# Kernel optimization log

Hardware: AMD Instinct MI355X
Metric: run time of the kernel (lower is better)

The kernel has to match this reference:

```python
import jax, jax.numpy as jnp
import numpy as np

EPS = 1e-5

def _layer_norm(x, g, b):
    mu = jnp.mean(x, axis=-1, keepdims=True)
    var = jnp.mean((x - mu) ** 2, axis=-1, keepdims=True)
    return (x - mu) * jax.lax.rsqrt(var + EPS) * g + b

def _aggregate(x, ei, emask):
    # x: [N, D], ei: [2, E], emask: [E] (0/1 float). Mean over valid incoming edges.
    N = x.shape[0]
    src, tgt = ei[0], ei[1]
    valid = emask > 0
    tgt_eff = jnp.where(valid, tgt, N)  # route masked edges to dummy segment
    msgs = x[src] * emask[:, None]      # [E, D]
    sums = jax.ops.segment_sum(msgs, tgt_eff, num_segments=N + 1)[:N]
    cnt = jax.ops.segment_sum(emask, tgt_eff, num_segments=N + 1)[:N]
    return sums / jnp.maximum(cnt, 1.0)[:, None]

def _forward(node_feats, edge_index, node_mask, edge_mask,
             in_W, in_b, self_W, self_b, neigh_W, neigh_b, ln_g, ln_b,
             out1_W, out1_b, out2_W, out2_b):
    x = jax.nn.relu(node_feats @ in_W + in_b)  # [B, N, H]
    L = self_W.shape[0]
    agg_fn = jax.vmap(_aggregate)
    for l in range(L):
        self_feats = x @ self_W[l] + self_b[l]
        neigh = agg_fn(x, edge_index, edge_mask)
        neigh_feats = neigh @ neigh_W[l] + neigh_b[l]
        h = jax.nn.relu(self_feats + neigh_feats)
        h = _layer_norm(h, ln_g[l], ln_b[l])
        x = h * node_mask[:, :, None]
    # global mean_max pool
    masked = x * node_mask[:, :, None]
    n_valid = jnp.maximum(jnp.sum(node_mask, axis=1, keepdims=True), 1.0)
    mean_pool = jnp.sum(masked, axis=1) / n_valid
    neg_inf = jnp.asarray(-jnp.inf, x.dtype)
    max_pool = jnp.max(jnp.where(node_mask[:, :, None] > 0, masked, neg_inf), axis=1)
    g = jnp.concatenate([mean_pool, max_pool], axis=1)  # [B, 2H]
    h = jax.nn.relu(g @ out1_W + out1_b)
    return h @ out2_W + out2_b  # [B, output_dim]

def setup_inputs() -> dict:
    key = jax.random.key(0)
    ks = jax.random.split(key, 12)
    B, N, E = 8, 8192, 65536
    F_IN, H, OUT, L = 64, 128, 256, 3
    inp = {}
    inp['graph_node_feats'] = jax.random.normal(ks[0], (B, N, F_IN), jnp.float32)
    inp['graph_edge_index'] = jax.random.randint(ks[1], (B, 2, E), 0, N, jnp.int32)
    inp['graph_node_mask'] = jnp.ones((B, N), jnp.float32)
    inp['graph_edge_mask'] = jnp.ones((B, E), jnp.float32)
    s = lambda k, sh, fan: jax.random.normal(k, sh, jnp.float32) * (1.0 / np.sqrt(fan))
    inp['in_W'] = s(ks[2], (F_IN, H), F_IN)
    inp['in_b'] = jnp.zeros((H,), jnp.float32)
    inp['self_W'] = s(ks[3], (L, H, H), H)
    inp['self_b'] = jnp.zeros((L, H), jnp.float32)
    inp['neigh_W'] = s(ks[4], (L, H, H), H)
    inp['neigh_b'] = jnp.zeros((L, H), jnp.float32)
    inp['ln_g'] = jnp.ones((L, H), jnp.float32)
    inp['ln_b'] = jnp.zeros((L, H), jnp.float32)
    inp['out1_W'] = s(ks[5], (2 * H, H), 2 * H)
    inp['out1_b'] = jnp.zeros((H,), jnp.float32)
    inp['out2_W'] = s(ks[6], (H, OUT), H)
    inp['out2_b'] = jnp.zeros((OUT,), jnp.float32)
    return inp

def reference(graph_node_feats, graph_edge_index, graph_node_mask, graph_edge_mask,
              in_W, in_b, self_W, self_b, neigh_W, neigh_b, ln_g, ln_b,
              out1_W, out1_b, out2_W, out2_b):
    return _forward(graph_node_feats, graph_edge_index, graph_node_mask, graph_edge_mask,
                    in_W, in_b, self_W, self_b, neigh_W, neigh_b, ln_g, ln_b,
                    out1_W, out1_b, out2_W, out2_b)
```

## Files before the change

kernel.cpp:

```cpp
#include <hip/hip_runtime.h>
#include <hip/hip_bf16.h>

#define B 8
#define N 8192
#define E 65536
#define FIN 64
#define H 128
#define OUTD 256
#define NLAYER 3
#define EPS 1e-5f
#define NCHUNK 128
#define NNODE (B * N)
#define KSTEPS 8
#define BPL (KSTEPS * 8 * 512)
#define INSTEPS 6
#define ELLW 48

#define AS1 __attribute__((address_space(1)))
#define AS3 __attribute__((address_space(3)))

typedef float f32x4 __attribute__((ext_vector_type(4)));
typedef __bf16 bf16x8 __attribute__((ext_vector_type(8)));

__device__ __forceinline__ float b2f(unsigned short u) {
    union { float f; unsigned int i; } c; c.i = ((unsigned int)u) << 16; return c.f;
}
__device__ __forceinline__ unsigned short f2b(float f) {
    __hip_bfloat16 h = __float2bfloat16(f);
    return *reinterpret_cast<unsigned short*>(&h);
}

__global__ void k_prep(const float* __restrict__ selfW, const float* __restrict__ neighW,
                       const float* __restrict__ inW,
                       unsigned short* __restrict__ Bp, unsigned short* __restrict__ Bpi) {
    const int idx = blockIdx.x;
    const int lane = threadIdx.x;
    const int quad = lane >> 4, col = lane & 15;
    if (idx < NLAYER * KSTEPS * 8) {
        const int t = idx & 7;
        const int s = (idx >> 3) % KSTEPS;
        const int l = idx / (KSTEPS * 8);
        const int g = s >> 2;
        const float* W = ((g == 0) ? selfW : neighW) + (size_t)l * H * H;
        const int n = t * 16 + col;
        unsigned short* dst = Bp + ((size_t)(l * KSTEPS + s) * 8 + t) * 512 + lane * 8;
        #pragma unroll
        for (int j = 0; j < 8; ++j) {
            const int kk = (s & 3) * 32 + quad * 8 + j;
            dst[j] = f2b(W[kk * H + n]);
        }
    } else {
        const int idx2 = idx - NLAYER * KSTEPS * 8;
        const int t = idx2 & 7;
        const int s = idx2 >> 3;
        const int g = s >> 1;
        const bool lo = (g == 2);
        const int n = t * 16 + col;
        unsigned short* dst = Bpi + ((size_t)(s * 8 + t)) * 512 + lane * 8;
        #pragma unroll
        for (int j = 0; j < 8; ++j) {
            const int kk = (s & 1) * 32 + quad * 8 + j;
            const float w = inW[kk * H + n];
            const unsigned short hi = f2b(w);
            dst[j] = lo ? f2b(w - b2f(hi)) : hi;
        }
    }
}

__global__ __launch_bounds__(256) void k_front(const float* __restrict__ feats,
                                               const unsigned short* __restrict__ Bpi,
                                               const float* __restrict__ bias,
                                               unsigned short* __restrict__ xh,
                                               const int* __restrict__ ei,
                                               const float* __restrict__ emask,
                                               int* __restrict__ ecnt,
                                               unsigned int* __restrict__ ell) {
    const int tid = threadIdx.x;
    if (blockIdx.x >= 1024) {
        const int ge = (blockIdx.x - 1024) * 256 + tid;
        const float m = emask[ge];
        if (m > 0.f) {
            const int b = ge >> 16, e = ge & 0xFFFF;
            const int tgt = ei[(b * 2 + 1) * E + e];
            const int src = ei[(b * 2) * E + e];
            const int r = b * N + tgt;
            const int p = atomicAdd(&ecnt[r], 1);
            if (p < ELLW)
                ell[(size_t)r * ELLW + p] = ((unsigned int)f2b(m) << 16) | (unsigned int)src;
        }
        return;
    }
    const int wv = tid >> 6, lane = tid & 63;
    const int quad = lane >> 4, col = lane & 15;
    const int mg = wv >> 1, nw = wv & 1;
    const int row0 = blockIdx.x * 64;

    bf16x8 fh[2][2], fl[2][2];
    #pragma unroll
    for (int mt = 0; mt < 2; ++mt) {
        const int row = row0 + (mg * 2 + mt) * 16 + col;
        #pragma unroll
        for (int j = 0; j < 2; ++j) {
            const float* src = &feats[(size_t)row * FIN + j * 32 + quad * 8];
            const float4 v0 = *(const float4*)src;
            const float4 v1 = *(const float4*)(src + 4);
            const float fv[8] = {v0.x, v0.y, v0.z, v0.w, v1.x, v1.y, v1.z, v1.w};
            union { bf16x8 v; unsigned short u[8]; } Hh, Ll;
            #pragma unroll
            for (int q = 0; q < 8; ++q) {
                const unsigned short hu = f2b(fv[q]);
                Hh.u[q] = hu;
                Ll.u[q] = f2b(fv[q] - b2f(hu));
            }
            fh[mt][j] = Hh.v;
            fl[mt][j] = Ll.v;
        }
    }

    f32x4 acc[2][4] = {};
    bf16x8 bC[4];
    #pragma unroll
    for (int nt = 0; nt < 4; ++nt)
        bC[nt] = *(const bf16x8*)&Bpi[((size_t)(nw * 4 + nt)) * 512 + lane * 8];

    #pragma unroll
    for (int s = 0; s < INSTEPS; ++s) {
        bf16x8 bN[4];
        if (s + 1 < INSTEPS) {
            #pragma unroll
            for (int nt = 0; nt < 4; ++nt)
                bN[nt] = *(const bf16x8*)&Bpi[((size_t)(s + 1) * 8 + nw * 4 + nt) * 512 + lane * 8];
        }
        const int g = s >> 1, j = s & 1;
        #pragma unroll
        for (int mt = 0; mt < 2; ++mt) {
            const bf16x8 a = (g == 1) ? fl[mt][j] : fh[mt][j];
            #pragma unroll
            for (int nt = 0; nt < 4; ++nt)
                acc[mt][nt] = __builtin_amdgcn_mfma_f32_16x16x32_bf16(a, bC[nt], acc[mt][nt], 0, 0, 0);
        }
        #pragma unroll
        for (int nt = 0; nt < 4; ++nt) bC[nt] = bN[nt];
    }

    #pragma unroll
    for (int nt = 0; nt < 4; ++nt) {
        const int hh = (nw * 4 + nt) * 16 + col;
        const float bv = bias[hh];
        #pragma unroll
        for (int mt = 0; mt < 2; ++mt)
            #pragma unroll
            for (int r = 0; r < 4; ++r) {
                const int row = row0 + (mg * 2 + mt) * 16 + quad * 4 + r;
                const float y = fmaxf(acc[mt][nt][r] + bv, 0.f);
                xh[(size_t)row * H + hh] = f2b(y);
            }
    }
}

__global__ __launch_bounds__(256) void k_gather7(const unsigned int* __restrict__ xh32,
                                                 const int* __restrict__ ecnt,
                                                 const unsigned int* __restrict__ ell,
                                                 unsigned int* __restrict__ nh32) {
    const int beta = blockIdx.x;
    const int b = beta & 7;
    const int grp = beta >> 3;
    const int wave = threadIdx.x >> 6, lane = threadIdx.x & 63;
    const int r = b * N + grp * 4 + wave;
    unsigned int pv = 0;
    if (lane < ELLW) pv = ell[(size_t)r * ELLW + lane];
    const int cnt = min(ecnt[r], ELLW);
    if (lane >= cnt) pv = 0;
    const size_t bbase = (size_t)b * N * 64;
    float a0 = 0.f, a1 = 0.f, c = 0.f;
    const int cnt8 = (cnt + 7) & ~7;
    for (int jj = 0; jj < cnt8; jj += 8) {
        #pragma unroll
        for (int q = 0; q < 8; ++q) {
            const unsigned int pk = __shfl(pv, jj + q);
            const float m = b2f((unsigned short)(pk >> 16));
            const unsigned int u = xh32[bbase + (size_t)(pk & 0xFFFFu) * 64 + lane];
            union { unsigned int i; float f; } lo, hi;
            lo.i = u << 16;
            hi.i = u & 0xFFFF0000u;
            a0 = fmaf(lo.f, m, a0);
            a1 = fmaf(hi.f, m, a1);
            c += m;
        }
    }
    const float inv = 1.f / fmaxf(c, 1.f);
    nh32[(size_t)r * 64 + lane] = (unsigned int)f2b(a0 * inv) | ((unsigned int)f2b(a1 * inv) << 16);
}

__global__ __launch_bounds__(256) void k_layer9(const unsigned short* __restrict__ xinh,
                                                const unsigned short* __restrict__ nh,
                                                const unsigned short* __restrict__ Bp,
                                                const float* __restrict__ sb,
                                                const float* __restrict__ nb,
                                                const float* __restrict__ lng,
                                                const float* __restrict__ lnb,
                                                const float* __restrict__ nmask,
                                                unsigned short* __restrict__ oxh,
                                                float* __restrict__ part,
                                                const int last) {
    __shared__ __align__(16) unsigned short bbuf[2][16 * 512];
    __shared__ float lsum[2][64];
    __shared__ float lsq[2][64];
    __shared__ float psum_s[2][H];
    __shared__ float pmax_s[2][H];

    const int tid = threadIdx.x;
    const int wv = tid >> 6, lane = tid & 63;
    const int quad = lane >> 4, col = lane & 15;
    const int mg = wv >> 1, nw = wv & 1;
    const int u = blockIdx.x;
    const int b = u & 7;
    const int chunk = u >> 3;
    const int row0 = b * N + chunk * 64;

    size_t abase[2];
    #pragma unroll
    for (int mt = 0; mt < 2; ++mt)
        abase[mt] = (size_t)(row0 + (mg * 2 + mt) * 16 + col) * H + quad * 8;

    #pragma unroll
    for (int i = 0; i < 4; ++i) {
        const unsigned short* g = Bp + (size_t)(wv * 4 + i) * 512 + lane * 8;
        __builtin_amdgcn_global_load_lds((const AS1 unsigned int*)g,
                                         (AS3 unsigned int*)&bbuf[0][(wv * 4 + i) * 512],
                                         16, 0, 0);
    }
    bf16x8 aC[2][2];
    #pragma unroll
    for (int j = 0; j < 2; ++j)
        #pragma unroll
        for (int mt = 0; mt < 2; ++mt)
            aC[j][mt] = *(const bf16x8*)&xinh[abase[mt] + j * 32];

    f32x4 acc[2][4] = {};

    #pragma unroll
    for (int c = 0; c < 4; ++c) {
        __syncthreads();
        bf16x8 aN[2][2];
        if (c < 3) {
            const int c1 = c + 1;
            #pragma unroll
            for (int i = 0; i < 4; ++i) {
                const unsigned short* g = Bp + (size_t)(c1 * 16 + wv * 4 + i) * 512 + lane * 8;
                __builtin_amdgcn_global_load_lds((const AS1 unsigned int*)g,
                                                 (AS3 unsigned int*)&bbuf[c1 & 1][(wv * 4 + i) * 512],
                                                 16, 0, 0);
            }
            const unsigned short* A1 = (c1 < 2) ? xinh : nh;
            #pragma unroll
            for (int j = 0; j < 2; ++j)
                #pragma unroll
                for (int mt = 0; mt < 2; ++mt)
                    aN[j][mt] = *(const bf16x8*)&A1[abase[mt] + ((c1 & 1) * 2 + j) * 32];
        }
        #pragma unroll
        for (int j = 0; j < 2; ++j) {
            bf16x8 bf[4];
            #pragma unroll
            for (int nt = 0; nt < 4; ++nt)
                bf[nt] = *(const bf16x8*)&bbuf[c & 1][(j * 8 + nw * 4 + nt) * 512 + lane * 8];
            #pragma unroll
            for (int mt = 0; mt < 2; ++mt)
                #pragma unroll
                for (int nt = 0; nt < 4; ++nt)
                    acc[mt][nt] = __builtin_amdgcn_mfma_f32_16x16x32_bf16(aC[j][mt], bf[nt], acc[mt][nt], 0, 0, 0);
        }
        #pragma unroll
        for (int j = 0; j < 2; ++j)
            #pragma unroll
            for (int mt = 0; mt < 2; ++mt)
                aC[j][mt] = aN[j][mt];
    }

    float sbv[4], nbv[4], gv[4], bbv[4];
    #pragma unroll
    for (int nt = 0; nt < 4; ++nt) {
        const int hh = (nw * 4 + nt) * 16 + col;
        sbv[nt] = sb[hh]; nbv[nt] = nb[hh]; gv[nt] = lng[hh]; bbv[nt] = lnb[hh];
    }
    #pragma unroll
    for (int mt = 0; mt < 2; ++mt)
        #pragma unroll
        for (int nt = 0; nt < 4; ++nt)
            #pragma unroll
            for (int r = 0; r < 4; ++r)
                acc[mt][nt][r] = fmaxf(acc[mt][nt][r] + sbv[nt] + nbv[nt], 0.f);

    #pragma unroll
    for (int mt = 0; mt < 2; ++mt)
        #pragma unroll
        for (int r = 0; r < 4; ++r) {
            float p = 0.f, q = 0.f;
            #pragma unroll
            for (int nt = 0; nt < 4; ++nt) {
                const float v = acc[mt][nt][r];
                p += v;
                q = fmaf(v, v, q);
            }
            p += __shfl_xor(p, 1);  q += __shfl_xor(q, 1);
            p += __shfl_xor(p, 2);  q += __shfl_xor(q, 2);
            p += __shfl_xor(p, 4);  q += __shfl_xor(q, 4);
            p += __shfl_xor(p, 8);  q += __shfl_xor(q, 8);
            if (col == 0) {
                const int rib = (mg * 2 + mt) * 16 + quad * 4 + r;
                lsum[nw][rib] = p;
                lsq[nw][rib] = q;
            }
        }
    __syncthreads();

    float psum[4] = {0.f, 0.f, 0.f, 0.f};
    float pmax[4] = {-INFINITY, -INFINITY, -INFINITY, -INFINITY};

    #pragma unroll
    for (int mt = 0; mt < 2; ++mt)
        #pragma unroll
        for (int r = 0; r < 4; ++r) {
            const int rib = (mg * 2 + mt) * 16 + quad * 4 + r;
            const int node = row0 + rib;
            const float mu = (lsum[0][rib] + lsum[1][rib]) * (1.f / H);
            const float var = (lsq[0][rib] + lsq[1][rib]) * (1.f / H) - mu * mu;
            const float isd = rsqrtf(var + EPS);
            const float m = nmask[node];
            #pragma unroll
            for (int nt = 0; nt < 4; ++nt) {
                const float y = (fmaf(acc[mt][nt][r] - mu, isd * gv[nt], bbv[nt])) * m;
                if (!last) {
                    oxh[(size_t)node * H + (nw * 4 + nt) * 16 + col] = f2b(y);
                } else {
                    psum[nt] += y;
                    pmax[nt] = fmaxf(pmax[nt], (m > 0.f) ? y : -INFINITY);
                }
            }
        }

    if (last) {
        #pragma unroll
        for (int nt = 0; nt < 4; ++nt) {
            psum[nt] += __shfl_xor(psum[nt], 16);
            psum[nt] += __shfl_xor(psum[nt], 32);
            pmax[nt] = fmaxf(pmax[nt], __shfl_xor(pmax[nt], 16));
            pmax[nt] = fmaxf(pmax[nt], __shfl_xor(pmax[nt], 32));
        }
        if (quad == 0)
            #pragma unroll
            for (int nt = 0; nt < 4; ++nt) {
                psum_s[mg][(nw * 4 + nt) * 16 + col] = psum[nt];
                pmax_s[mg][(nw * 4 + nt) * 16 + col] = pmax[nt];
            }
        float nv = 0.f;
        if (wv == 0) {
            nv = nmask[row0 + lane];
            nv += __shfl_xor(nv, 1);  nv += __shfl_xor(nv, 2);
            nv += __shfl_xor(nv, 4);  nv += __shfl_xor(nv, 8);
            nv += __shfl_xor(nv, 16); nv += __shfl_xor(nv, 32);
        }
        __syncthreads();
        float* p = part + ((size_t)b * NCHUNK + chunk) * (2 * H + 1);
        if (tid < H) {
            p[tid] = psum_s[0][tid] + psum_s[1][tid];
            p[H + tid] = fmaxf(pmax_s[0][tid], pmax_s[1][tid]);
        }
        if (tid == 0) p[2 * H] = nv;
    }
}

__global__ __launch_bounds__(1024) void k_tail2(const float* __restrict__ part,
                                                const float* __restrict__ W1, const float* __restrict__ b1,
                                                const float* __restrict__ W2, const float* __restrict__ b2,
                                                float* __restrict__ out) {
    const int b = blockIdx.x, tid = threadIdx.x;
    const int col = tid & 255;
    const int sub = tid >> 8;
    __shared__ float sred[4][2 * H];
    __shared__ float nvl[NCHUNK];
    __shared__ float g[2 * H];
    __shared__ float hid[H];

    {
        float acc = (col < H) ? 0.f : -INFINITY;
        #pragma unroll 8
        for (int c = sub * (NCHUNK / 4); c < (sub + 1) * (NCHUNK / 4); ++c) {
            const float v = part[((size_t)b * NCHUNK + c) * (2 * H + 1) + col];
            acc = (col < H) ? (acc + v) : fmaxf(acc, v);
        }
        sred[sub][col] = acc;
    }
    if (tid < NCHUNK)
        nvl[tid] = part[((size_t)b * NCHUNK + tid) * (2 * H + 1) + 2 * H];
    __syncthreads();
    for (int s = NCHUNK / 2; s > 0; s >>= 1) {
        if (tid < s) nvl[tid] += nvl[tid + s];
        __syncthreads();
    }
    const float nv = fmaxf(nvl[0], 1.f);
    if (tid < 2 * H) {
        if (tid < H)
            g[tid] = (sred[0][tid] + sred[1][tid] + sred[2][tid] + sred[3][tid]) / nv;
        else
            g[tid] = fmaxf(fmaxf(sred[0][tid], sred[1][tid]), fmaxf(sred[2][tid], sred[3][tid]));
    }
    __syncthreads();
    if (tid < H) {
        float a = b1[tid];
        #pragma unroll 8
        for (int k = 0; k < 2 * H; ++k) a = fmaf(g[k], W1[k * H + tid], a);
        hid[tid] = fmaxf(a, 0.f);
    }
    __syncthreads();
    if (tid < OUTD) {
        float a = b2[tid];
        #pragma unroll 8
        for (int k = 0; k < H; ++k) a = fmaf(hid[k], W2[k * OUTD + tid], a);
        out[(size_t)b * OUTD + tid] = a;
    }
}

extern "C" void kernel_launch(void* const* d_in, const int* in_sizes, int n_in,
                              void* d_out, int out_size, void* d_ws, size_t ws_size,
                              hipStream_t stream) {
    const float* feats = (const float*)d_in[0];
    const int*   ei    = (const int*)d_in[1];
    const float* nmask = (const float*)d_in[2];
    const float* emask = (const float*)d_in[3];
    const float* inW   = (const float*)d_in[4];
    const float* inb   = (const float*)d_in[5];
    const float* selfW = (const float*)d_in[6];
    const float* selfb = (const float*)d_in[7];
    const float* neighW= (const float*)d_in[8];
    const float* neighb= (const float*)d_in[9];
    const float* lng   = (const float*)d_in[10];
    const float* lnb   = (const float*)d_in[11];
    const float* W1    = (const float*)d_in[12];
    const float* b1    = (const float*)d_in[13];
    const float* W2    = (const float*)d_in[14];
    const float* b2    = (const float*)d_in[15];
    float* out = (float*)d_out;

    const size_t nxh = (size_t)NNODE * H;
    char* w = (char*)d_ws;
    unsigned short* xh  = (unsigned short*)w;  w += nxh * 2;
    unsigned short* nh  = (unsigned short*)w;  w += nxh * 2;
    unsigned short* Bp  = (unsigned short*)w;  w += (size_t)NLAYER * BPL * 2;
    unsigned short* Bpi = (unsigned short*)w;  w += (size_t)INSTEPS * 8 * 512 * 2;
    float* part = (float*)w;                   w += (size_t)B * NCHUNK * (2 * H + 1) * 4;
    int* ecnt   = (int*)w;                     w += (size_t)NNODE * 4;
    unsigned int* ell = (unsigned int*)w;      w += (size_t)NNODE * ELLW * 4;

    k_prep<<<NLAYER * KSTEPS * 8 + INSTEPS * 8, 64, 0, stream>>>(selfW, neighW, inW, Bp, Bpi);
    hipMemsetAsync(ecnt, 0, (size_t)NNODE * sizeof(int), stream);
    k_front<<<1024 + B * E / 256, 256, 0, stream>>>(feats, Bpi, inb, xh, ei, emask, ecnt, ell);

    for (int l = 0; l < NLAYER; ++l) {
        k_gather7<<<NNODE / 4, 256, 0, stream>>>((const unsigned int*)xh, ecnt, ell,
                                                 (unsigned int*)nh);
        k_layer9<<<NNODE / 64, 256, 0, stream>>>(xh, nh,
                                                 Bp + (size_t)l * BPL,
                                                 selfb + (size_t)l * H, neighb + (size_t)l * H,
                                                 lng + (size_t)l * H, lnb + (size_t)l * H,
                                                 nmask, xh, part, (l == NLAYER - 1) ? 1 : 0);
    }

    k_tail2<<<B, 1024, 0, stream>>>(part, W1, b1, W2, b2, out);
}
```

Before: 253.1 us.

## Fuse whole GNN pipeline into one persistent cooperative kernel with grid syncs

Replaces the separate prep, front, per-layer gather and layer kernels and the tail kernel with one cooperative persistent kernel. Work items are assigned to blocks with grid-stride loops, and phases are separated by grid.sync. The aim is to remove kernel launch gaps and the memset. In exchange it adds grid-wide barrier cost, caps occupancy through launch bounds, and serialises the front GEMM and ELL build inside each block; the old multi-kernel path stays as a fallback.

Result: slower. 906.6 us (+258.2%).

```diff
diff --git a/kernel.cpp b/kernel.cpp
--- a/kernel.cpp
+++ b/kernel.cpp
@@ -1,5 +1,8 @@
 #include <hip/hip_runtime.h>
 #include <hip/hip_bf16.h>
+#include <hip/hip_cooperative_groups.h>
+
+namespace cg = cooperative_groups;
 
 #define B 8
 #define N 8192
@@ -30,6 +33,366 @@
     return *reinterpret_cast<unsigned short*>(&h);
 }
 
+struct MegaArgs {
+    const float *feats; const int *ei; const float *nmask; const float *emask;
+    const float *inW, *inb, *selfW, *selfb, *neighW, *neighb, *lng, *lnb;
+    const float *W1, *b1, *W2, *b2;
+    float *out;
+    unsigned short *xh, *nh, *Bp, *Bpi;
+    float *part, *part2;
+    int *ecnt; unsigned int *ell;
+};
+
+__global__ __launch_bounds__(256, 4) void k_mega(MegaArgs A) {
+    cg::grid_group grid = cg::this_grid();
+    __shared__ __align__(16) unsigned short bbuf[2][16 * 512];
+    __shared__ float lsum[2][64], lsq[2][64];
+    __shared__ float psum_s[2][H], pmax_s[2][H];
+
+    const int bid = blockIdx.x, tid = threadIdx.x, GD = gridDim.x;
+    const int wv = tid >> 6, lane = tid & 63;
+    const int quad = lane >> 4, col = lane & 15;
+
+    for (int i = bid * 256 + tid; i < NNODE; i += GD * 256) A.ecnt[i] = 0;
+    for (int u4 = bid; u4 < 60; u4 += GD) {
+        const int idx = u4 * 4 + wv;
+        if (idx < NLAYER * KSTEPS * 8) {
+            const int t = idx & 7;
+            const int s = (idx >> 3) % KSTEPS;
+            const int l = idx / (KSTEPS * 8);
+            const float* W = (((s >> 2) == 0) ? A.selfW : A.neighW) + (size_t)l * H * H;
+            const int n = t * 16 + col;
+            unsigned short* dst = A.Bp + ((size_t)(l * KSTEPS + s) * 8 + t) * 512 + lane * 8;
+            #pragma unroll
+            for (int j = 0; j < 8; ++j)
+                dst[j] = f2b(W[((s & 3) * 32 + quad * 8 + j) * H + n]);
+        } else {
+            const int idx2 = idx - NLAYER * KSTEPS * 8;
+            const int t = idx2 & 7;
+            const int s = idx2 >> 3;
+            const bool lo = ((s >> 1) == 2);
+            const int n = t * 16 + col;
+            unsigned short* dst = A.Bpi + ((size_t)(s * 8 + t)) * 512 + lane * 8;
+            #pragma unroll
+            for (int j = 0; j < 8; ++j) {
+                const float w = A.inW[((s & 1) * 32 + quad * 8 + j) * H + n];
+                const unsigned short hi = f2b(w);
+                dst[j] = lo ? f2b(w - b2f(hi)) : hi;
+            }
+        }
+    }
+    grid.sync();
+
+    for (int u = bid; u < NNODE / 64; u += GD) {
+        const int mg = wv >> 1, nw = wv & 1;
+        const int row0 = u * 64;
+        bf16x8 fh[2][2], fl[2][2];
+        #pragma unroll
+        for (int mt = 0; mt < 2; ++mt) {
+            const int row = row0 + (mg * 2 + mt) * 16 + col;
+            #pragma unroll
+            for (int j = 0; j < 2; ++j) {
+                const float* src = &A.feats[(size_t)row * FIN + j * 32 + quad * 8];
+                const float4 v0 = *(const float4*)src;
+                const float4 v1 = *(const float4*)(src + 4);
+                const float fv[8] = {v0.x, v0.y, v0.z, v0.w, v1.x, v1.y, v1.z, v1.w};
+                union { bf16x8 v; unsigned short u16[8]; } Hh, Ll;
+                #pragma unroll
+                for (int q = 0; q < 8; ++q) {
+                    const unsigned short hu = f2b(fv[q]);
+                    Hh.u16[q] = hu;
+                    Ll.u16[q] = f2b(fv[q] - b2f(hu));
+                }
+                fh[mt][j] = Hh.v;
+                fl[mt][j] = Ll.v;
+            }
+        }
+        f32x4 acc[2][4] = {};
+        bf16x8 bC[4];
+        #pragma unroll
+        for (int nt = 0; nt < 4; ++nt)
+            bC[nt] = *(const bf16x8*)&A.Bpi[((size_t)(nw * 4 + nt)) * 512 + lane * 8];
+        #pragma unroll
+        for (int s = 0; s < INSTEPS; ++s) {
+            bf16x8 bN[4];
+            if (s + 1 < INSTEPS) {
+                #pragma unroll
+                for (int nt = 0; nt < 4; ++nt)
+                    bN[nt] = *(const bf16x8*)&A.Bpi[((size_t)(s + 1) * 8 + nw * 4 + nt) * 512 + lane * 8];
+            }
+            const int g = s >> 1, j = s & 1;
+            #pragma unroll
+            for (int mt = 0; mt < 2; ++mt) {
+                const bf16x8 a = (g == 1) ? fl[mt][j] : fh[mt][j];
+                #pragma unroll
+                for (int nt = 0; nt < 4; ++nt)
+                    acc[mt][nt] = __builtin_amdgcn_mfma_f32_16x16x32_bf16(a, bC[nt], acc[mt][nt], 0, 0, 0);
+            }
+            #pragma unroll
+            for (int nt = 0; nt < 4; ++nt) bC[nt] = bN[nt];
+        }
+        #pragma unroll
+        for (int nt = 0; nt < 4; ++nt) {
+            const int hh = (nw * 4 + nt) * 16 + col;
+            const float bv = A.inb[hh];
+            #pragma unroll
+            for (int mt = 0; mt < 2; ++mt)
+                #pragma unroll
+                for (int r = 0; r < 4; ++r) {
+                    const int row = row0 + (mg * 2 + mt) * 16 + quad * 4 + r;
+                    A.xh[(size_t)row * H + hh] = f2b(fmaxf(acc[mt][nt][r] + bv, 0.f));
+                }
+        }
+    }
+    for (int u = bid; u < (B * E) / 256; u += GD) {
+        const int ge = u * 256 + tid;
+        const float m = A.emask[ge];
+        if (m > 0.f) {
+            const int b = ge >> 16, e = ge & 0xFFFF;
+            const int tgt = A.ei[(b * 2 + 1) * E + e];
+            const int src = A.ei[(b * 2) * E + e];
+            const int r = b * N + tgt;
+            const int p = atomicAdd(&A.ecnt[r], 1);
+            if (p < ELLW)
+                A.ell[(size_t)r * ELLW + p] = ((unsigned int)f2b(m) << 16) | (unsigned int)src;
+        }
+    }
+    grid.sync();
+
+    const unsigned int* xh32 = (const unsigned int*)A.xh;
+    unsigned int* nh32 = (unsigned int*)A.nh;
+    for (int l = 0; l < NLAYER; ++l) {
+        for (int q = bid; q < NNODE / 4; q += GD) {
+            const int b = q & 7;
+            const int r = b * N + (q >> 3) * 4 + wv;
+            unsigned int pv = 0;
+            if (lane < ELLW) pv = A.ell[(size_t)r * ELLW + lane];
+            const int cnt = min(A.ecnt[r], ELLW);
+            if (lane >= cnt) pv = 0;
+            const size_t bbase = (size_t)b * N * 64;
+            float a0 = 0.f, a1 = 0.f, c = 0.f;
+            const int cnt8 = (cnt + 7) & ~7;
+            for (int jj = 0; jj < cnt8; jj += 8) {
+                #pragma unroll
+                for (int qq = 0; qq < 8; ++qq) {
+                    const unsigned int pk = __shfl(pv, jj + qq);
+                    const float m = b2f((unsigned short)(pk >> 16));
+                    const unsigned int uu = xh32[bbase + (size_t)(pk & 0xFFFFu) * 64 + lane];
+                    union { unsigned int i; float f; } lo, hi;
+                    lo.i = uu << 16;
+                    hi.i = uu & 0xFFFF0000u;
+                    a0 = fmaf(lo.f, m, a0);
+                    a1 = fmaf(hi.f, m, a1);
+                    c += m;
+                }
+            }
+            const float inv = 1.f / fmaxf(c, 1.f);
+            nh32[(size_t)r * 64 + lane] = (unsigned int)f2b(a0 * inv) | ((unsigned int)f2b(a1 * inv) << 16);
+        }
+        grid.sync();
+
+        const unsigned short* Bpl = A.Bp + (size_t)l * BPL;
+        const float* sb = A.selfb + l * H;
+        const float* nb = A.neighb + l * H;
+        const float* lg = A.lng + l * H;
+        const float* lb = A.lnb + l * H;
+        const int last = (l == NLAYER - 1);
+        for (int u = bid; u < NNODE / 64; u += GD) {
+            const int mg = wv >> 1, nw = wv & 1;
+            const int b = u & 7;
+            const int chunk = u >> 3;
+            const int row0 = b * N + chunk * 64;
+            size_t abase[2];
+            #pragma unroll
+            for (int mt = 0; mt < 2; ++mt)
+                abase[mt] = (size_t)(row0 + (mg * 2 + mt) * 16 + col) * H + quad * 8;
+            #pragma unroll
+            for (int i = 0; i < 4; ++i) {
+                const unsigned short* g = Bpl + (size_t)(wv * 4 + i) * 512 + lane * 8;
+                __builtin_amdgcn_global_load_lds((const AS1 unsigned int*)g,
+                                                 (AS3 unsigned int*)&bbuf[0][(wv * 4 + i) * 512],
+                                                 16, 0, 0);
+            }
+            bf16x8 aC[2][2];
+            #pragma unroll
+            for (int j = 0; j < 2; ++j)
+                #pragma unroll
+                for (int mt = 0; mt < 2; ++mt)
+                    aC[j][mt] = *(const bf16x8*)&A.xh[abase[mt] + j * 32];
+            f32x4 acc[2][4] = {};
+            #pragma unroll
+            for (int c = 0; c < 4; ++c) {
+                __syncthreads();
+                bf16x8 aN[2][2];
+                if (c < 3) {
+                    const int c1 = c + 1;
+                    #pragma unroll
+                    for (int i = 0; i < 4; ++i) {
+                        const unsigned short* g = Bpl + (size_t)(c1 * 16 + wv * 4 + i) * 512 + lane * 8;
+                        __builtin_amdgcn_global_load_lds((const AS1 unsigned int*)g,
+                                                         (AS3 unsigned int*)&bbuf[c1 & 1][(wv * 4 + i) * 512],
+                                                         16, 0, 0);
+                    }
+                    const unsigned short* A1 = (c1 < 2) ? A.xh : A.nh;
+                    #pragma unroll
+                    for (int j = 0; j < 2; ++j)
+                        #pragma unroll
+                        for (int mt = 0; mt < 2; ++mt)
+                            aN[j][mt] = *(const bf16x8*)&A1[abase[mt] + ((c1 & 1) * 2 + j) * 32];
+                }
+                #pragma unroll
+                for (int j = 0; j < 2; ++j) {
+                    bf16x8 bf[4];
+                    #pragma unroll
+                    for (int nt = 0; nt < 4; ++nt)
+                        bf[nt] = *(const bf16x8*)&bbuf[c & 1][(j * 8 + nw * 4 + nt) * 512 + lane * 8];
+                    #pragma unroll
+                    for (int mt = 0; mt < 2; ++mt)
+                        #pragma unroll
+                        for (int nt = 0; nt < 4; ++nt)
+                            acc[mt][nt] = __builtin_amdgcn_mfma_f32_16x16x32_bf16(aC[j][mt], bf[nt], acc[mt][nt], 0, 0, 0);
+                }
+                #pragma unroll
+                for (int j = 0; j < 2; ++j)
+                    #pragma unroll
+                    for (int mt = 0; mt < 2; ++mt)
+                        aC[j][mt] = aN[j][mt];
+            }
+            float sbv[4], nbv[4], gv[4], bbv[4];
+            #pragma unroll
+            for (int nt = 0; nt < 4; ++nt) {
+                const int hh = (nw * 4 + nt) * 16 + col;
+                sbv[nt] = sb[hh]; nbv[nt] = nb[hh]; gv[nt] = lg[hh]; bbv[nt] = lb[hh];
+            }
+            #pragma unroll
+            for (int mt = 0; mt < 2; ++mt)
+                #pragma unroll
+                for (int nt = 0; nt < 4; ++nt)
+                    #pragma unroll
+                    for (int r = 0; r < 4; ++r)
+                        acc[mt][nt][r] = fmaxf(acc[mt][nt][r] + sbv[nt] + nbv[nt], 0.f);
+            #pragma unroll
+            for (int mt = 0; mt < 2; ++mt)
+                #pragma unroll
+                for (int r = 0; r < 4; ++r) {
+                    float p = 0.f, q = 0.f;
+                    #pragma unroll
+                    for (int nt = 0; nt < 4; ++nt) {
+                        const float v = acc[mt][nt][r];
+                        p += v;
+                        q = fmaf(v, v, q);
+                    }
+                    p += __shfl_xor(p, 1);  q += __shfl_xor(q, 1);
+                    p += __shfl_xor(p, 2);  q += __shfl_xor(q, 2);
+                    p += __shfl_xor(p, 4);  q += __shfl_xor(q, 4);
+                    p += __shfl_xor(p, 8);  q += __shfl_xor(q, 8);
+                    if (col == 0) {
+                        const int rib = (mg * 2 + mt) * 16 + quad * 4 + r;
+                        lsum[nw][rib] = p;
+                        lsq[nw][rib] = q;
+                    }
+                }
+            __syncthreads();
+            float psum[4] = {0.f, 0.f, 0.f, 0.f};
+            float pmax[4] = {-INFINITY, -INFINITY, -INFINITY, -INFINITY};
+            #pragma unroll
+            for (int mt = 0; mt < 2; ++mt)
+                #pragma unroll
+                for (int r = 0; r < 4; ++r) {
+                    const int rib = (mg * 2 + mt) * 16 + quad * 4 + r;
+                    const int node = row0 + rib;
+                    const float mu = (lsum[0][rib] + lsum[1][rib]) * (1.f / H);
+                    const float var = (lsq[0][rib] + lsq[1][rib]) * (1.f / H) - mu * mu;
+                    const float isd = rsqrtf(var + EPS);
+                    const float m = A.nmask[node];
+                    #pragma unroll
+                    for (int nt = 0; nt < 4; ++nt) {
+                        const float y = (fmaf(acc[mt][nt][r] - mu, isd * gv[nt], bbv[nt])) * m;
+                        if (!last) {
+                            A.xh[(size_t)node * H + (nw * 4 + nt) * 16 + col] = f2b(y);
+                        } else {
+                            psum[nt] += y;
+                            pmax[nt] = fmaxf(pmax[nt], (m > 0.f) ? y : -INFINITY);
+                        }
+                    }
+                }
+            if (last) {
+                #pragma unroll
+                for (int nt = 0; nt < 4; ++nt) {
+                    psum[nt] += __shfl_xor(psum[nt], 16);
+                    psum[nt] += __shfl_xor(psum[nt], 32);
+                    pmax[nt] = fmaxf(pmax[nt], __shfl_xor(pmax[nt], 16));
+                    pmax[nt] = fmaxf(pmax[nt], __shfl_xor(pmax[nt], 32));
+                }
+                if (quad == 0)
+                    #pragma unroll
+                    for (int nt = 0; nt < 4; ++nt) {
+                        psum_s[mg][(nw * 4 + nt) * 16 + col] = psum[nt];
+                        pmax_s[mg][(nw * 4 + nt) * 16 + col] = pmax[nt];
+                    }
+                float nv = 0.f;
+                if (wv == 0) {
+                    nv = A.nmask[row0 + lane];
+                    nv += __shfl_xor(nv, 1);  nv += __shfl_xor(nv, 2);
+                    nv += __shfl_xor(nv, 4);  nv += __shfl_xor(nv, 8);
+                    nv += __shfl_xor(nv, 16); nv += __shfl_xor(nv, 32);
+                }
+                __syncthreads();
+                float* p = A.part + ((size_t)b * NCHUNK + chunk) * (2 * H + 1);
+                if (tid < H) {
+                    p[tid] = psum_s[0][tid] + psum_s[1][tid];
+                    p[H + tid] = fmaxf(pmax_s[0][tid], pmax_s[1][tid]);
+                }
+                if (tid == 0) p[2 * H] = nv;
+            }
+        }
+        grid.sync();
+    }
+
+    if (bid < 32) {
+        const int b = bid >> 2, sub = bid & 3;
+        float acc = (tid < H) ? 0.f : -INFINITY;
+        float nv = 0.f;
+        for (int c = sub * (NCHUNK / 4); c < (sub + 1) * (NCHUNK / 4); ++c) {
+            const float* p = A.part + ((size_t)b * NCHUNK + c) * (2 * H + 1);
+            if (tid < H) acc += p[tid];
+            else acc = fmaxf(acc, p[tid]);
+            if (tid == 0) nv += p[2 * H];
+        }
+        float* q = A.part2 + (size_t)(b * 4 + sub) * 258;
+        q[tid] = acc;
+        if (tid == 0) q[256] = nv;
+    }
+    grid.sync();
+
+    if (bid < 8) {
+        const int b = bid;
+        float* g = (float*)&bbuf[0][0];
+        float* hid = g + 272;
+        const float* q0 = A.part2 + (size_t)(b * 4 + 0) * 258;
+        const float* q1 = A.part2 + (size_t)(b * 4 + 1) * 258;
+        const float* q2 = A.part2 + (size_t)(b * 4 + 2) * 258;
+        const float* q3 = A.part2 + (size_t)(b * 4 + 3) * 258;
+        const float nv = fmaxf(q0[256] + q1[256] + q2[256] + q3[256], 1.f);
+        if (tid < H)
+            g[tid] = (q0[tid] + q1[tid] + q2[tid] + q3[tid]) / nv;
+        else
+            g[tid] = fmaxf(fmaxf(q0[tid], q1[tid]), fmaxf(q2[tid], q3[tid]));
+        __syncthreads();
+        if (tid < H) {
+            float a = A.b1[tid];
+            #pragma unroll 8
+            for (int k = 0; k < 2 * H; ++k) a = fmaf(g[k], A.W1[k * H + tid], a);
+            hid[tid] = fmaxf(a, 0.f);
+        }
+        __syncthreads();
+        float a = A.b2[tid];
+        #pragma unroll 8
+        for (int k = 0; k < H; ++k) a = fmaf(hid[k], A.W2[k * OUTD + tid], a);
+        A.out[(size_t)b * OUTD + tid] = a;
+    }
+}
+
 __global__ void k_prep(const float* __restrict__ selfW, const float* __restrict__ neighW,
                        const float* __restrict__ inW,
                        unsigned short* __restrict__ Bp, unsigned short* __restrict__ Bpi) {
@@ -40,27 +403,22 @@
         const int t = idx & 7;
         const int s = (idx >> 3) % KSTEPS;
         const int l = idx / (KSTEPS * 8);
-        const int g = s >> 2;
-        const float* W = ((g == 0) ? selfW : neighW) + (size_t)l * H * H;
+        const float* W = (((s >> 2) == 0) ? selfW : neighW) + (size_t)l * H * H;
         const int n = t * 16 + col;
         unsigned short* dst = Bp + ((size_t)(l * KSTEPS + s) * 8 + t) * 512 + lane * 8;
         #pragma unroll
-        for (int j = 0; j < 8; ++j) {
-            const int kk = (s & 3) * 32 + quad * 8 + j;
-            dst[j] = f2b(W[kk * H + n]);
-        }
+        for (int j = 0; j < 8; ++j)
+            dst[j] = f2b(W[((s & 3) * 32 + quad * 8 + j) * H + n]);
     } else {
         const int idx2 = idx - NLAYER * KSTEPS * 8;
         const int t = idx2 & 7;
         const int s = idx2 >> 3;
-        const int g = s >> 1;
-        const bool lo = (g == 2);
+        const bool lo = ((s >> 1) == 2);
         const int n = t * 16 + col;
         unsigned short* dst = Bpi + ((size_t)(s * 8 + t)) * 512 + lane * 8;
         #pragma unroll
         for (int j = 0; j < 8; ++j) {
-            const int kk = (s & 1) * 32 + quad * 8 + j;
-            const float w = inW[kk * H + n];
+            const float w = inW[((s & 1) * 32 + quad * 8 + j) * H + n];
             const unsigned short hi = f2b(w);
             dst[j] = lo ? f2b(w - b2f(hi)) : hi;
         }
@@ -94,7 +452,6 @@
     const int quad = lane >> 4, col = lane & 15;
     const int mg = wv >> 1, nw = wv & 1;
     const int row0 = blockIdx.x * 64;
-
     bf16x8 fh[2][2], fl[2][2];
     #pragma unroll
     for (int mt = 0; mt < 2; ++mt) {
@@ -116,13 +473,11 @@
             fl[mt][j] = Ll.v;
         }
     }
-
     f32x4 acc[2][4] = {};
     bf16x8 bC[4];
     #pragma unroll
     for (int nt = 0; nt < 4; ++nt)
         bC[nt] = *(const bf16x8*)&Bpi[((size_t)(nw * 4 + nt)) * 512 + lane * 8];
-
     #pragma unroll
     for (int s = 0; s < INSTEPS; ++s) {
         bf16x8 bN[4];
@@ -142,7 +497,6 @@
         #pragma unroll
         for (int nt = 0; nt < 4; ++nt) bC[nt] = bN[nt];
     }
-
     #pragma unroll
     for (int nt = 0; nt < 4; ++nt) {
         const int hh = (nw * 4 + nt) * 16 + col;
@@ -152,8 +506,7 @@
             #pragma unroll
             for (int r = 0; r < 4; ++r) {
                 const int row = row0 + (mg * 2 + mt) * 16 + quad * 4 + r;
-                const float y = fmaxf(acc[mt][nt][r] + bv, 0.f);
-                xh[(size_t)row * H + hh] = f2b(y);
+                xh[(size_t)row * H + hh] = f2b(fmaxf(acc[mt][nt][r] + bv, 0.f));
             }
     }
 }
@@ -208,7 +561,6 @@
     __shared__ float lsq[2][64];
     __shared__ float psum_s[2][H];
     __shared__ float pmax_s[2][H];
-
     const int tid = threadIdx.x;
     const int wv = tid >> 6, lane = tid & 63;
     const int quad = lane >> 4, col = lane & 15;
@@ -217,12 +569,10 @@
     const int b = u & 7;
     const int chunk = u >> 3;
     const int row0 = b * N + chunk * 64;
-
     size_t abase[2];
     #pragma unroll
     for (int mt = 0; mt < 2; ++mt)
         abase[mt] = (size_t)(row0 + (mg * 2 + mt) * 16 + col) * H + quad * 8;
-
     #pragma unroll
     for (int i = 0; i < 4; ++i) {
         const unsigned short* g = Bp + (size_t)(wv * 4 + i) * 512 + lane * 8;
@@ -236,9 +586,7 @@
         #pragma unroll
         for (int mt = 0; mt < 2; ++mt)
             aC[j][mt] = *(const bf16x8*)&xinh[abase[mt] + j * 32];
-
     f32x4 acc[2][4] = {};
-
     #pragma unroll
     for (int c = 0; c < 4; ++c) {
         __syncthreads();
@@ -277,7 +625,6 @@
             for (int mt = 0; mt < 2; ++mt)
                 aC[j][mt] = aN[j][mt];
     }
-
     float sbv[4], nbv[4], gv[4], bbv[4];
     #pragma unroll
     for (int nt = 0; nt < 4; ++nt) {
@@ -291,7 +638,6 @@
             #pragma unroll
             for (int r = 0; r < 4; ++r)
                 acc[mt][nt][r] = fmaxf(acc[mt][nt][r] + sbv[nt] + nbv[nt], 0.f);
-
     #pragma unroll
     for (int mt = 0; mt < 2; ++mt)
         #pragma unroll
@@ -314,10 +660,8 @@
             }
         }
     __syncthreads();
-
     float psum[4] = {0.f, 0.f, 0.f, 0.f};
     float pmax[4] = {-INFINITY, -INFINITY, -INFINITY, -INFINITY};
-
     #pragma unroll
     for (int mt = 0; mt < 2; ++mt)
         #pragma unroll
@@ -339,7 +683,6 @@
                 }
             }
         }
-
     if (last) {
         #pragma unroll
         for (int nt = 0; nt < 4; ++nt) {
@@ -382,7 +725,6 @@
     __shared__ float nvl[NCHUNK];
     __shared__ float g[2 * H];
     __shared__ float hid[H];
-
     {
         float acc = (col < H) ? 0.f : -INFINITY;
         #pragma unroll 8
@@ -449,14 +791,37 @@
     unsigned short* nh  = (unsigned short*)w;  w += nxh * 2;
     unsigned short* Bp  = (unsigned short*)w;  w += (size_t)NLAYER * BPL * 2;
     unsigned short* Bpi = (unsigned short*)w;  w += (size_t)INSTEPS * 8 * 512 * 2;
-    float* part = (float*)w;                   w += (size_t)B * NCHUNK * (2 * H + 1) * 4;
+    float* part  = (float*)w;                  w += (size_t)B * NCHUNK * (2 * H + 1) * 4;
+    float* part2 = (float*)w;                  w += (size_t)32 * 258 * 4;
     int* ecnt   = (int*)w;                     w += (size_t)NNODE * 4;
     unsigned int* ell = (unsigned int*)w;      w += (size_t)NNODE * ELLW * 4;
+
+    int maxB = 0;
+    hipError_t qerr = hipOccupancyMaxActiveBlocksPerMultiprocessor(&maxB, k_mega, 256, 0);
+    int grid = (qerr == hipSuccess) ? maxB * 256 : 0;
+    if (grid > 1024) grid = 1024;
+    grid &= ~7;
+    bool coop = (grid >= 64);
+    if (coop) {
+        MegaArgs A;
+        A.feats = feats; A.ei = ei; A.nmask = nmask; A.emask = emask;
+        A.inW = inW; A.inb = inb; A.selfW = selfW; A.selfb = selfb;
+        A.neighW = neighW; A.neighb = neighb; A.lng = lng; A.lnb = lnb;
+        A.W1 = W1; A.b1 = b1; A.W2 = W2; A.b2 = b2;
+        A.out = out;
+        A.xh = xh; A.nh = nh; A.Bp = Bp; A.Bpi = Bpi;
+        A.part = part; A.part2 = part2;
+        A.ecnt = ecnt; A.ell = ell;
+        void* kargs[] = {&A};
+        hipError_t err = hipLaunchCooperativeKernel((const void*)k_mega, dim3(grid), dim3(256),
+                                                    kargs, 0, stream);
+        coop = (err == hipSuccess);
+    }
+    if (coop) return;
 
     k_prep<<<NLAYER * KSTEPS * 8 + INSTEPS * 8, 64, 0, stream>>>(selfW, neighW, inW, Bp, Bpi);
     hipMemsetAsync(ecnt, 0, (size_t)NNODE * sizeof(int), stream);
     k_front<<<1024 + B * E / 256, 256, 0, stream>>>(feats, Bpi, inb, xh, ei, emask, ecnt, ell);
-
     for (int l = 0; l < NLAYER; ++l) {
         k_gather7<<<NNODE / 4, 256, 0, stream>>>((const unsigned int*)xh, ecnt, ell,
                                                  (unsigned int*)nh);
@@ -466,6 +831,5 @@
                                                  lng + (size_t)l * H, lnb + (size_t)l * H,
                                                  nmask, xh, part, (l == NLAYER - 1) ? 1 : 0);
     }
-
     k_tail2<<<B, 1024, 0, stream>>>(part, W1, b1, W2, b2, out);
 }
```

## Fuse pooling tail into last layer kernel and memset into prep kernel

Applied to the files above, without the earlier changes.

Moves the zeroing of the edge counters into extra blocks of the weight-prep kernel, which removes the separate memset call. The final pooling and MLP head is folded into the last layer kernel. Each block increments a global ticket counter, and the last eight blocks spin until every block has finished, then each computes one graph's head. This saves two launches, but the last blocks must wait in a spin loop and run the head on 256 threads instead of 1024. It also depends on forward-progress assumptions for the spinning blocks.

Result: slower. 338.0 us (+33.6%).

```diff
diff --git a/kernel.cpp b/kernel.cpp
--- a/kernel.cpp
+++ b/kernel.cpp
@@ -15,6 +15,8 @@
 #define BPL (KSTEPS * 8 * 512)
 #define INSTEPS 6
 #define ELLW 48
+#define PREPN (NLAYER * KSTEPS * 8 + INSTEPS * 8)
+#define LGRID (NNODE / 64)
 
 #define AS1 __attribute__((address_space(1)))
 #define AS3 __attribute__((address_space(3)))
@@ -32,35 +34,36 @@
 
 __global__ void k_prep(const float* __restrict__ selfW, const float* __restrict__ neighW,
                        const float* __restrict__ inW,
-                       unsigned short* __restrict__ Bp, unsigned short* __restrict__ Bpi) {
+                       unsigned short* __restrict__ Bp, unsigned short* __restrict__ Bpi,
+                       int* __restrict__ ecnt, int* __restrict__ ctr) {
     const int idx = blockIdx.x;
     const int lane = threadIdx.x;
     const int quad = lane >> 4, col = lane & 15;
+    if (idx >= PREPN) {
+        ecnt[(idx - PREPN) * 64 + lane] = 0;
+        if (idx == PREPN && lane == 0) *ctr = 0;
+        return;
+    }
     if (idx < NLAYER * KSTEPS * 8) {
         const int t = idx & 7;
         const int s = (idx >> 3) % KSTEPS;
         const int l = idx / (KSTEPS * 8);
-        const int g = s >> 2;
-        const float* W = ((g == 0) ? selfW : neighW) + (size_t)l * H * H;
+        const float* W = (((s >> 2) == 0) ? selfW : neighW) + (size_t)l * H * H;
         const int n = t * 16 + col;
         unsigned short* dst = Bp + ((size_t)(l * KSTEPS + s) * 8 + t) * 512 + lane * 8;
         #pragma unroll
-        for (int j = 0; j < 8; ++j) {
-            const int kk = (s & 3) * 32 + quad * 8 + j;
-            dst[j] = f2b(W[kk * H + n]);
-        }
+        for (int j = 0; j < 8; ++j)
+            dst[j] = f2b(W[((s & 3) * 32 + quad * 8 + j) * H + n]);
     } else {
         const int idx2 = idx - NLAYER * KSTEPS * 8;
         const int t = idx2 & 7;
         const int s = idx2 >> 3;
-        const int g = s >> 1;
-        const bool lo = (g == 2);
+        const bool lo = ((s >> 1) == 2);
         const int n = t * 16 + col;
         unsigned short* dst = Bpi + ((size_t)(s * 8 + t)) * 512 + lane * 8;
         #pragma unroll
         for (int j = 0; j < 8; ++j) {
-            const int kk = (s & 1) * 32 + quad * 8 + j;
-            const float w = inW[kk * H + n];
+            const float w = inW[((s & 1) * 32 + quad * 8 + j) * H + n];
             const unsigned short hi = f2b(w);
             dst[j] = lo ? f2b(w - b2f(hi)) : hi;
         }
@@ -94,7 +97,6 @@
     const int quad = lane >> 4, col = lane & 15;
     const int mg = wv >> 1, nw = wv & 1;
     const int row0 = blockIdx.x * 64;
-
     bf16x8 fh[2][2], fl[2][2];
     #pragma unroll
     for (int mt = 0; mt < 2; ++mt) {
@@ -116,13 +118,11 @@
             fl[mt][j] = Ll.v;
         }
     }
-
     f32x4 acc[2][4] = {};
     bf16x8 bC[4];
     #pragma unroll
     for (int nt = 0; nt < 4; ++nt)
         bC[nt] = *(const bf16x8*)&Bpi[((size_t)(nw * 4 + nt)) * 512 + lane * 8];
-
     #pragma unroll
     for (int s = 0; s < INSTEPS; ++s) {
         bf16x8 bN[4];
@@ -142,7 +142,6 @@
         #pragma unroll
         for (int nt = 0; nt < 4; ++nt) bC[nt] = bN[nt];
     }
-
     #pragma unroll
     for (int nt = 0; nt < 4; ++nt) {
         const int hh = (nw * 4 + nt) * 16 + col;
@@ -152,8 +151,7 @@
             #pragma unroll
             for (int r = 0; r < 4; ++r) {
                 const int row = row0 + (mg * 2 + mt) * 16 + quad * 4 + r;
-                const float y = fmaxf(acc[mt][nt][r] + bv, 0.f);
-                xh[(size_t)row * H + hh] = f2b(y);
+                xh[(size_t)row * H + hh] = f2b(fmaxf(acc[mt][nt][r] + bv, 0.f));
             }
     }
 }
@@ -192,22 +190,28 @@
     nh32[(size_t)r * 64 + lane] = (unsigned int)f2b(a0 * inv) | ((unsigned int)f2b(a1 * inv) << 16);
 }
 
-__global__ __launch_bounds__(256) void k_layer9(const unsigned short* __restrict__ xinh,
-                                                const unsigned short* __restrict__ nh,
-                                                const unsigned short* __restrict__ Bp,
-                                                const float* __restrict__ sb,
-                                                const float* __restrict__ nb,
-                                                const float* __restrict__ lng,
-                                                const float* __restrict__ lnb,
-                                                const float* __restrict__ nmask,
-                                                unsigned short* __restrict__ oxh,
-                                                float* __restrict__ part,
-                                                const int last) {
+__global__ __launch_bounds__(256) void k_layer10(const unsigned short* __restrict__ xinh,
+                                                 const unsigned short* __restrict__ nh,
+                                                 const unsigned short* __restrict__ Bp,
+                                                 const float* __restrict__ sb,
+                                                 const float* __restrict__ nb,
+                                                 const float* __restrict__ lng,
+                                                 const float* __restrict__ lnb,
+                                                 const float* __restrict__ nmask,
+                                                 unsigned short* __restrict__ oxh,
+                                                 float* __restrict__ part,
+                                                 const float* __restrict__ W1, const float* __restrict__ b1,
+                                                 const float* __restrict__ W2, const float* __restrict__ b2,
+                                                 float* __restrict__ out,
+                                                 int* __restrict__ ctr,
+                                                 const int last) {
     __shared__ __align__(16) unsigned short bbuf[2][16 * 512];
     __shared__ float lsum[2][64];
     __shared__ float lsq[2][64];
     __shared__ float psum_s[2][H];
     __shared__ float pmax_s[2][H];
+    __shared__ float nvl[NCHUNK];
+    __shared__ int tick_s;
 
     const int tid = threadIdx.x;
     const int wv = tid >> 6, lane = tid & 63;
@@ -340,28 +344,30 @@
             }
         }
 
-    if (last) {
+    if (!last) return;
+
+    #pragma unroll
+    for (int nt = 0; nt < 4; ++nt) {
+        psum[nt] += __shfl_xor(psum[nt], 16);
+        psum[nt] += __shfl_xor(psum[nt], 32);
+        pmax[nt] = fmaxf(pmax[nt], __shfl_xor(pmax[nt], 16));
+        pmax[nt] = fmaxf(pmax[nt], __shfl_xor(pmax[nt], 32));
+    }
+    if (quad == 0)
         #pragma unroll
         for (int nt = 0; nt < 4; ++nt) {
-            psum[nt] += __shfl_xor(psum[nt], 16);
-            psum[nt] += __shfl_xor(psum[nt], 32);
-            pmax[nt] = fmaxf(pmax[nt], __shfl_xor(pmax[nt], 16));
-            pmax[nt] = fmaxf(pmax[nt], __shfl_xor(pmax[nt], 32));
-        }
-        if (quad == 0)
-            #pragma unroll
-            for (int nt = 0; nt < 4; ++nt) {
-                psum_s[mg][(nw * 4 + nt) * 16 + col] = psum[nt];
-                pmax_s[mg][(nw * 4 + nt) * 16 + col] = pmax[nt];
-            }
-        float nv = 0.f;
-        if (wv == 0) {
-            nv = nmask[row0 + lane];
-            nv += __shfl_xor(nv, 1);  nv += __shfl_xor(nv, 2);
-            nv += __shfl_xor(nv, 4);  nv += __shfl_xor(nv, 8);
-            nv += __shfl_xor(nv, 16); nv += __shfl_xor(nv, 32);
-        }
-        __syncthreads();
+            psum_s[mg][(nw * 4 + nt) * 16 + col] = psum[nt];
+            pmax_s[mg][(nw * 4 + nt) * 16 + col] = pmax[nt];
+        }
+    float nv = 0.f;
+    if (wv == 0) {
+        nv = nmask[row0 + lane];
+        nv += __shfl_xor(nv, 1);  nv += __shfl_xor(nv, 2);
+        nv += __shfl_xor(nv, 4);  nv += __shfl_xor(nv, 8);
+        nv += __shfl_xor(nv, 16); nv += __shfl_xor(nv, 32);
+    }
+    __syncthreads();
+    {
         float* p = part + ((size_t)b * NCHUNK + chunk) * (2 * H + 1);
         if (tid < H) {
             p[tid] = psum_s[0][tid] + psum_s[1][tid];
@@ -369,43 +375,35 @@
         }
         if (tid == 0) p[2 * H] = nv;
     }
-}
-
-__global__ __launch_bounds__(1024) void k_tail2(const float* __restrict__ part,
-                                                const float* __restrict__ W1, const float* __restrict__ b1,
-                                                const float* __restrict__ W2, const float* __restrict__ b2,
-                                                float* __restrict__ out) {
-    const int b = blockIdx.x, tid = threadIdx.x;
-    const int col = tid & 255;
-    const int sub = tid >> 8;
-    __shared__ float sred[4][2 * H];
-    __shared__ float nvl[NCHUNK];
-    __shared__ float g[2 * H];
-    __shared__ float hid[H];
-
-    {
-        float acc = (col < H) ? 0.f : -INFINITY;
-        #pragma unroll 8
-        for (int c = sub * (NCHUNK / 4); c < (sub + 1) * (NCHUNK / 4); ++c) {
-            const float v = part[((size_t)b * NCHUNK + c) * (2 * H + 1) + col];
-            acc = (col < H) ? (acc + v) : fmaxf(acc, v);
-        }
-        sred[sub][col] = acc;
+
+    __threadfence();
+    if (tid == 0) tick_s = atomicAdd(ctr, 1);
+    __syncthreads();
+    const int tick = tick_s;
+    if (tick < LGRID - 8) return;
+    if (tid == 0) {
+        while (atomicAdd(ctr, 0) < LGRID) { __builtin_amdgcn_s_sleep(8); }
+    }
+    __syncthreads();
+    __threadfence();
+    const int bb = tick - (LGRID - 8);
+
+    float accv = (tid < H) ? 0.f : -INFINITY;
+    for (int c = 0; c < NCHUNK; ++c) {
+        const float v = part[((size_t)bb * NCHUNK + c) * (2 * H + 1) + tid];
+        accv = (tid < H) ? (accv + v) : fmaxf(accv, v);
     }
     if (tid < NCHUNK)
-        nvl[tid] = part[((size_t)b * NCHUNK + tid) * (2 * H + 1) + 2 * H];
+        nvl[tid] = part[((size_t)bb * NCHUNK + tid) * (2 * H + 1) + 2 * H];
     __syncthreads();
     for (int s = NCHUNK / 2; s > 0; s >>= 1) {
         if (tid < s) nvl[tid] += nvl[tid + s];
         __syncthreads();
     }
-    const float nv = fmaxf(nvl[0], 1.f);
-    if (tid < 2 * H) {
-        if (tid < H)
-            g[tid] = (sred[0][tid] + sred[1][tid] + sred[2][tid] + sred[3][tid]) / nv;
-        else
-            g[tid] = fmaxf(fmaxf(sred[0][tid], sred[1][tid]), fmaxf(sred[2][tid], sred[3][tid]));
-    }
+    const float nv2 = fmaxf(nvl[0], 1.f);
+    float* g = &psum_s[0][0];
+    float* hid = &pmax_s[0][0];
+    g[tid] = (tid < H) ? accv / nv2 : accv;
     __syncthreads();
     if (tid < H) {
         float a = b1[tid];
@@ -414,12 +412,10 @@
         hid[tid] = fmaxf(a, 0.f);
     }
     __syncthreads();
-    if (tid < OUTD) {
-        float a = b2[tid];
-        #pragma unroll 8
-        for (int k = 0; k < H; ++k) a = fmaf(hid[k], W2[k * OUTD + tid], a);
-        out[(size_t)b * OUTD + tid] = a;
-    }
+    float a = b2[tid];
+    #pragma unroll 8
+    for (int k = 0; k < H; ++k) a = fmaf(hid[k], W2[k * OUTD + tid], a);
+    out[(size_t)bb * OUTD + tid] = a;
 }
 
 extern "C" void kernel_launch(void* const* d_in, const int* in_sizes, int n_in,
@@ -451,21 +447,21 @@
     unsigned short* Bpi = (unsigned short*)w;  w += (size_t)INSTEPS * 8 * 512 * 2;
     float* part = (float*)w;                   w += (size_t)B * NCHUNK * (2 * H + 1) * 4;
     int* ecnt   = (int*)w;                     w += (size_t)NNODE * 4;
+    int* ctr    = (int*)w;                     w += 16;
     unsigned int* ell = (unsigned int*)w;      w += (size_t)NNODE * ELLW * 4;
 
-    k_prep<<<NLAYER * KSTEPS * 8 + INSTEPS * 8, 64, 0, stream>>>(selfW, neighW, inW, Bp, Bpi);
-    hipMemsetAsync(ecnt, 0, (size_t)NNODE * sizeof(int), stream);
+    k_prep<<<PREPN + NNODE / 64, 64, 0, stream>>>(selfW, neighW, inW, Bp, Bpi, ecnt, ctr);
     k_front<<<1024 + B * E / 256, 256, 0, stream>>>(feats, Bpi, inb, xh, ei, emask, ecnt, ell);
 
     for (int l = 0; l < NLAYER; ++l) {
         k_gather7<<<NNODE / 4, 256, 0, stream>>>((const unsigned int*)xh, ecnt, ell,
                                                  (unsigned int*)nh);
-        k_layer9<<<NNODE / 64, 256, 0, stream>>>(xh, nh,
-                                                 Bp + (size_t)l * BPL,
-                                                 selfb + (size_t)l * H, neighb + (size_t)l * H,
-                                                 lng + (size_t)l * H, lnb + (size_t)l * H,
-                                                 nmask, xh, part, (l == NLAYER - 1) ? 1 : 0);
-    }
-
-    k_tail2<<<B, 1024, 0, stream>>>(part, W1, b1, W2, b2, out);
-}
+        k_layer10<<<LGRID, 256, 0, stream>>>(xh, nh,
+                                             Bp + (size_t)l * BPL,
+                                             selfb + (size_t)l * H, neighb + (size_t)l * H,
+                                             lng + (size_t)l * H, lnb + (size_t)l * H,
+                                             nmask, xh, part,
+                                             W1, b1, W2, b2, out, ctr,
+                                             (l == NLAYER - 1) ? 1 : 0);
+    }
+}
```
